# Performance work log

Hardware: AMD Instinct MI355X
Metric: run time of the kernel (lower is better)

Reference implementation:

```python
import jax, jax.numpy as jnp
import numpy as np
import math

PHI = (1.0 + math.sqrt(5.0)) / 2.0
LN_EPS = 1e-5


def _carrier_phases(n_heads: int) -> np.ndarray:
    """Reproduce DimensionalHeadManager._allocate carrier phases."""
    base = [k * math.pi / 7.0 for k in range(7)]  # rung base phases
    n_rungs = 7
    raw = []
    remaining = n_heads
    for i in range(n_rungs):
        if i < n_rungs - 1:
            c = max(1, round(n_heads / PHI ** (i + 1)))
            c = min(c, remaining - (n_rungs - 1 - i))
            raw.append(c)
            remaining -= c
        else:
            raw.append(max(1, remaining))
    phases = []
    for rung_idx, count in enumerate(raw):
        for j in range(count):
            phases.append(base[rung_idx] + 2.0 * math.pi / max(count, 1) * j)
    return np.asarray(phases[:n_heads], dtype=np.float32)


def setup_inputs() -> dict:
    key = jax.random.key(0)
    ks = jax.random.split(key, 7)
    B, S, D, H = 2, 2048, 1024, 16
    w_scale = 0.02  # realistic init scale for Linear weights
    x = jax.random.normal(ks[0], (B, S, D), dtype=jnp.float32)
    Wq = jax.random.normal(ks[1], (D, D), dtype=jnp.float32) * w_scale
    Wk = jax.random.normal(ks[2], (D, D), dtype=jnp.float32) * w_scale
    Wv = jax.random.normal(ks[3], (D, D), dtype=jnp.float32) * w_scale
    Wo = jax.random.normal(ks[4], (D, D), dtype=jnp.float32) * w_scale
    Wp = jax.random.normal(ks[5], (D,), dtype=jnp.float32) * w_scale  # W_phase (1,D) flattened
    gamma = jnp.ones((D,), dtype=jnp.float32)
    beta = jnp.zeros((D,), dtype=jnp.float32)
    carrier = jnp.asarray(_carrier_phases(H))  # srl.carrier_freq init
    lam = jnp.float32(0.1)  # lambda_resonance init
    return {"x": x, "Wq": Wq, "Wk": Wk, "Wv": Wv, "Wo": Wo, "Wp": Wp,
            "gamma": gamma, "beta": beta, "carrier": carrier, "lam": lam}


def reference(x, Wq, Wk, Wv, Wo, Wp, gamma, beta, carrier, lam):
    B, S, D = x.shape
    H = carrier.shape[0]
    dh = D // H
    scale = 1.0 / math.sqrt(dh)

    residual = x
    # LayerNorm
    mu = jnp.mean(x, axis=-1, keepdims=True)
    var = jnp.mean((x - mu) ** 2, axis=-1, keepdims=True)
    xn = (x - mu) * jax.lax.rsqrt(var + LN_EPS) * gamma + beta

    # Q/K/V projections (torch Linear: y = x @ W.T), split into heads
    q = jnp.einsum('bsd,ed->bse', xn, Wq).reshape(B, S, H, dh)
    k = jnp.einsum('bsd,ed->bse', xn, Wk).reshape(B, S, H, dh)
    v = jnp.einsum('bsd,ed->bse', xn, Wv).reshape(B, S, H, dh)

    # scalar phase per token, per-head carrier resonance gate
    phase = jnp.einsum('bsd,d->bs', xn, Wp)                       # (B,S)
    head_T = jnp.cos((phase[..., None] - carrier) * 0.5) ** 2     # (B,S,H)

    # attention scores + resonance term R_ij = cos^2((phi_i - phi_j)/2)
    scores = jnp.einsum('bihd,bjhd->bhij', q, k) * scale          # (B,H,S,S)
    R = jnp.cos((phase[:, :, None] - phase[:, None, :]) * 0.5) ** 2  # (B,S,S)
    scores = scores + lam * R[:, None, :, :]

    attn = jax.nn.softmax(scores, axis=-1)
    out = jnp.einsum('bhij,bjhd->bihd', attn, v)                  # (B,S,H,dh)
    out = out * head_T[..., None]                                 # per-head resonance gating
    emergent_energy = jnp.sum(jnp.abs(out))
    y = residual + jnp.einsum('bse,de->bsd', out.reshape(B, S, D), Wo)
    return (y, emergent_energy)
```

## Files before the change

### kernel.cpp

```cpp
#include <hip/hip_runtime.h>
#include <hip/hip_bf16.h>

#define S_LEN 2048
#define D_MODEL 1024
#define NH 16
#define DH 64
#define M_TOK 4096
#define DK 80
#define JS 2

typedef __attribute__((ext_vector_type(8))) short bf16x8;
typedef __attribute__((ext_vector_type(4))) float f32x4;
typedef __attribute__((ext_vector_type(16))) float f32x16;

#define LOG2E 1.4426950408889634f

__device__ __forceinline__ unsigned short f2bf(float f) {
  unsigned u = __float_as_uint(f);
  u += 0x7FFF + ((u >> 16) & 1);
  return (unsigned short)(u >> 16);
}

__device__ __forceinline__ void gl16(const void* g, void* l) {
  __builtin_amdgcn_global_load_lds(
      (const __attribute__((address_space(1))) unsigned int*)g,
      (__attribute__((address_space(3))) unsigned int*)l, 16, 0, 0);
}

__device__ __forceinline__ void pl32swap(unsigned int& a, unsigned int& b) {
  asm volatile("v_permlane32_swap_b32 %0, %1" : "+v"(a), "+v"(b));
}

__global__ __launch_bounds__(256) void prep_kernel(
    const float* __restrict__ Wq, const float* __restrict__ Wk,
    const float* __restrict__ Wv, const float* __restrict__ Wo,
    unsigned short* __restrict__ wbf) {
  int idx = (blockIdx.x * 256 + threadIdx.x) * 4;
  int wsel = idx >> 20;
  const float* s = (wsel == 0) ? Wq : (wsel == 1) ? Wk : (wsel == 2) ? Wv : Wo;
  int off = idx & 1048575;
  float4 v = *(const float4*)(s + off);
  ushort4 p;
  p.x = f2bf(v.x); p.y = f2bf(v.y); p.z = f2bf(v.z); p.w = f2bf(v.w);
  *(ushort4*)(wbf + idx) = p;
}

__device__ __forceinline__ float block_sum(float v, float* sm) {
#pragma unroll
  for (int o = 32; o > 0; o >>= 1) v += __shfl_xor(v, o, 64);
  int w = threadIdx.x >> 6;
  __syncthreads();
  if ((threadIdx.x & 63) == 0) sm[w] = v;
  __syncthreads();
  return sm[0] + sm[1] + sm[2] + sm[3];
}

__global__ __launch_bounds__(256) void ln_phase_kernel(
    const float* __restrict__ x, const float* __restrict__ Wp,
    const float* __restrict__ gamma, const float* __restrict__ beta,
    unsigned short* __restrict__ xn, float* __restrict__ cosP,
    float* __restrict__ sinP, unsigned short* __restrict__ kk80) {
  __shared__ float sm[4];
  int row = blockIdx.x;
  int tid = threadIdx.x;
  float4 v = ((const float4*)(x + (size_t)row * D_MODEL))[tid];
  float mu = block_sum(v.x + v.y + v.z + v.w, sm) * (1.0f / D_MODEL);
  float d0 = v.x - mu, d1 = v.y - mu, d2 = v.z - mu, d3 = v.w - mu;
  float var = block_sum(d0 * d0 + d1 * d1 + d2 * d2 + d3 * d3, sm) * (1.0f / D_MODEL);
  float rinv = rsqrtf(var + 1e-5f);
  float4 g = ((const float4*)gamma)[tid];
  float4 be = ((const float4*)beta)[tid];
  float n0 = d0 * rinv * g.x + be.x;
  float n1 = d1 * rinv * g.y + be.y;
  float n2 = d2 * rinv * g.z + be.z;
  float n3 = d3 * rinv * g.w + be.w;
  ushort4 p;
  p.x = f2bf(n0); p.y = f2bf(n1); p.z = f2bf(n2); p.w = f2bf(n3);
  ((ushort4*)(xn + (size_t)row * D_MODEL))[tid] = p;
  float4 wp = ((const float4*)Wp)[tid];
  float ph = block_sum(n0 * wp.x + n1 * wp.y + n2 * wp.z + n3 * wp.w, sm);
  if (tid == 0) {
    cosP[row] = cosf(ph);
    sinP[row] = sinf(ph);
  }
  if (tid < 16) {
    float cp = cosf(ph), sp = sinf(ph);
    unsigned int w0 = (unsigned int)f2bf(cp) | ((unsigned int)f2bf(sp) << 16);
    int b_ = row >> 11, s_ = row & (S_LEN - 1);
    *(int4*)(kk80 + ((size_t)((b_ * NH + tid) * S_LEN + s_)) * DK + 64) =
        make_int4((int)w0, 0, 0, 0);
  }
}

__global__ __launch_bounds__(256, 3) void qkv_gemm_kernel(
    const unsigned short* __restrict__ xn, const unsigned short* __restrict__ wbf,
    unsigned short* __restrict__ q, unsigned short* __restrict__ kk80,
    unsigned short* __restrict__ vT) {
  __shared__ __align__(16) unsigned short As[128 * 64];
  __shared__ __align__(16) unsigned short Bs[128 * 64];
  int bid = blockIdx.x;
  bool vmode = bid >= 512;
  const unsigned short* Ap;
  const unsigned short* Bp;
  int m0, n0;
  if (!vmode) {
    m0 = (bid >> 4) * 128;
    n0 = (bid & 15) * 128;
    Ap = xn; Bp = wbf;
  } else {
    int v2 = bid - 512;
    m0 = (v2 & 7) * 128;
    n0 = (v2 >> 3) * 128;
    Ap = wbf + 2 * D_MODEL * D_MODEL; Bp = xn;
  }
  int tid = threadIdx.x;
  int wave = tid >> 6, lane = tid & 63, quad = lane >> 4, l15 = lane & 15;
  int wm = (wave & 1) * 64, wn = (wave >> 1) * 64;
  f32x4 acc[4][4];
#pragma unroll
  for (int r = 0; r < 4; ++r)
#pragma unroll
    for (int c = 0; c < 4; ++c) acc[r][c] = (f32x4){0.f, 0.f, 0.f, 0.f};

  for (int k0 = 0; k0 < D_MODEL; k0 += 64) {
    __syncthreads();
#pragma unroll
    for (int t = 0; t < 4; ++t) {
      int c = t * 256 + tid;
      int r = c >> 3, p = c & 7;
      int g = p ^ (r & 7);
      gl16(&Ap[(size_t)(m0 + r) * D_MODEL + k0 + g * 8], &As[c * 8]);
      gl16(&Bp[(size_t)(n0 + r) * D_MODEL + k0 + g * 8], &Bs[c * 8]);
    }
    __syncthreads();
    bf16x8 af[4][2], bfr[4][2];
#pragma unroll
    for (int r = 0; r < 4; ++r) {
      int R = wm + r * 16 + l15;
#pragma unroll
      for (int h = 0; h < 2; ++h)
        af[r][h] = *(const bf16x8*)&As[R * 64 + ((h * 4 + quad) ^ (R & 7)) * 8];
    }
#pragma unroll
    for (int c = 0; c < 4; ++c) {
      int R = wn + c * 16 + l15;
#pragma unroll
      for (int h = 0; h < 2; ++h)
        bfr[c][h] = *(const bf16x8*)&Bs[R * 64 + ((h * 4 + quad) ^ (R & 7)) * 8];
    }
#pragma unroll
    for (int h = 0; h < 2; ++h)
#pragma unroll
      for (int r = 0; r < 4; ++r)
#pragma unroll
        for (int c = 0; c < 4; ++c)
          acc[r][c] = __builtin_amdgcn_mfma_f32_16x16x32_bf16(af[r][h], bfr[c][h], acc[r][c], 0, 0, 0);
  }
#pragma unroll
  for (int r = 0; r < 4; ++r) {
#pragma unroll
    for (int c = 0; c < 4; ++c) {
#pragma unroll
      for (int rr = 0; rr < 4; ++rr) {
        if (vmode) {
          int e = m0 + wm + r * 16 + quad * 4 + rr;
          int tok = n0 + wn + c * 16 + l15;
          int hh = e >> 6, d = e & 63;
          int bb = tok >> 11, ss = tok & (S_LEN - 1);
          vT[(((size_t)(bb * NH + hh)) * DH + d) * S_LEN + ss] = f2bf(acc[r][c][rr]);
        } else {
          int tok = m0 + wm + r * 16 + quad * 4 + rr;
          int n = n0 + wn + c * 16 + l15;
          int e = n & 1023;
          int hh = e >> 6, d = e & 63;
          int bb = tok >> 11, ss = tok & (S_LEN - 1);
          if ((n0 >> 10) == 0) {
            q[(((size_t)(bb * NH + hh)) * S_LEN + ss) * DH + d] =
                f2bf(acc[r][c][rr] * (0.125f * LOG2E));
          } else {
            kk80[(((size_t)(bb * NH + hh)) * S_LEN + ss) * DK + d] = f2bf(acc[r][c][rr]);
          }
        }
      }
    }
  }
}

__global__ __launch_bounds__(128, 2) void attn_kernel(
    const unsigned short* __restrict__ q, const unsigned short* __restrict__ kk80,
    const unsigned short* __restrict__ vT, const float* __restrict__ cosP,
    const float* __restrict__ sinP, const float* __restrict__ lamp,
    float* __restrict__ Opart, float* __restrict__ lpart) {
  __shared__ __align__(16) unsigned short Ks[64 * 72];
  __shared__ __align__(16) unsigned short Vs[512 * 8];
  int xx = blockIdx.x;
  int qt = xx & 15, js = xx >> 4;
  int h = blockIdx.y, b = blockIdx.z;
  int bh = b * NH + h;
  int tid = threadIdx.x, wave = tid >> 6, lane = tid & 63;
  int half = lane >> 5, l31 = lane & 31;

  const unsigned short* kb = kk80 + (size_t)bh * S_LEN * DK;
  const unsigned short* vb = vT + (size_t)bh * DH * S_LEN;
  int i0 = qt * 128 + wave * 64;

  bf16x8 bQ0[5], bQ1[5];
  {
    float hl2 = 0.5f * lamp[0] * LOG2E;
#pragma unroll
    for (int si = 0; si < 2; ++si) {
      int qrow = i0 + si * 32 + l31;
      const unsigned short* qp = q + ((size_t)bh * S_LEN + qrow) * DH;
      bf16x8* dst = si ? bQ1 : bQ0;
#pragma unroll
      for (int db = 0; db < 4; ++db)
        dst[db] = *(const bf16x8*)(qp + db * 16 + half * 8);
      bf16x8 z8 = {0, 0, 0, 0, 0, 0, 0, 0};
      if (half == 0) {
        z8[0] = (short)f2bf(hl2 * cosP[b * S_LEN + qrow]);
        z8[1] = (short)f2bf(hl2 * sinP[b * S_LEN + qrow]);
      }
      dst[4] = z8;
    }
  }

  unsigned int cc0 = tid, cc1 = tid + 128, cc2 = tid + 256, cc3 = tid + 384,
               cc4 = tid + 512;
  unsigned int kr0 = cc0 / 9u, kr1 = cc1 / 9u, kr2 = cc2 / 9u, kr3 = cc3 / 9u,
               kr4 = cc4 / 9u;
  unsigned int ko0 = kr0 * DK + (cc0 - kr0 * 9u) * 8;
  unsigned int ko1 = kr1 * DK + (cc1 - kr1 * 9u) * 8;
  unsigned int ko2 = kr2 * DK + (cc2 - kr2 * 9u) * 8;
  unsigned int ko3 = kr3 * DK + (cc3 - kr3 * 9u) * 8;
  unsigned int ko4 = kr4 * DK + (cc4 - kr4 * 9u) * 8;
  unsigned short* kl0 = (unsigned short*)Ks + cc0 * 8;
  unsigned short* kl1 = (unsigned short*)Ks + cc1 * 8;
  unsigned short* kl2 = (unsigned short*)Ks + cc2 * 8;
  unsigned short* kl3 = (unsigned short*)Ks + cc3 * 8;
  unsigned short* kl4 = (unsigned short*)Ks + cc4 * 8;
  unsigned int vr0 = cc0 >> 3, vr1 = cc1 >> 3, vr2 = cc2 >> 3, vr3 = cc3 >> 3;
  unsigned int vo0 = vr0 * S_LEN + ((cc0 & 7) ^ (vr0 & 7)) * 8;
  unsigned int vo1 = vr1 * S_LEN + ((cc1 & 7) ^ (vr1 & 7)) * 8;
  unsigned int vo2 = vr2 * S_LEN + ((cc2 & 7) ^ (vr2 & 7)) * 8;
  unsigned int vo3 = vr3 * S_LEN + ((cc3 & 7) ^ (vr3 & 7)) * 8;
  unsigned short* vl0 = (unsigned short*)Vs + cc0 * 8;
  unsigned short* vl1 = (unsigned short*)Vs + cc1 * 8;
  unsigned short* vl2 = (unsigned short*)Vs + cc2 * 8;
  unsigned short* vl3 = (unsigned short*)Vs + cc3 * 8;

  const unsigned short* kbt = kb + (size_t)(js * (S_LEN / JS)) * DK;
  const unsigned short* vbt = vb + js * (S_LEN / JS);

  f32x16 O00 = {}, O01 = {}, O10 = {}, O11 = {};
  float li0 = 0.f, li1 = 0.f;

  for (int jt = 0; jt < S_LEN / (64 * JS); ++jt) {
    __syncthreads();
    gl16(kbt + ko0, kl0);
    gl16(kbt + ko1, kl1);
    gl16(kbt + ko2, kl2);
    gl16(kbt + ko3, kl3);
    if (tid < 64) gl16(kbt + ko4, kl4);
    gl16(vbt + vo0, vl0);
    gl16(vbt + vo1, vl1);
    gl16(vbt + vo2, vl2);
    gl16(vbt + vo3, vl3);
    kbt += 64 * DK;
    vbt += 64;
    __syncthreads();

#pragma unroll
    for (int sj = 0; sj < 2; ++sj) {
      f32x16 Sf0 = {}, Sf1 = {};
      int r = sj * 32 + l31;
      __builtin_amdgcn_s_setprio(1);
#pragma unroll
      for (int db = 0; db < 5; ++db) {
        int p = (db < 4) ? (db * 2 + half) : 8;
        bf16x8 aK = *(const bf16x8*)((const unsigned short*)Ks + (r * 9 + p) * 8);
        Sf0 = __builtin_amdgcn_mfma_f32_32x32x16_bf16(aK, bQ0[db], Sf0, 0, 0, 0);
        Sf1 = __builtin_amdgcn_mfma_f32_32x32x16_bf16(aK, bQ1[db], Sf1, 0, 0, 0);
      }
      __builtin_amdgcn_s_setprio(0);

      bf16x8 pa00, pa01, pa10, pa11;
      auto smx = [&](const f32x16& S, float& li, bf16x8& pu0, bf16x8& pu1) {
        unsigned int w[8];
#pragma unroll
        for (int rr = 0; rr < 8; ++rr) {
          float e0 = exp2f(S[rr * 2 + 0]);
          float e1 = exp2f(S[rr * 2 + 1]);
          li += e0 + e1;
          __hip_bfloat162 pk2 = __float22bfloat162_rn(float2{e0, e1});
          w[rr] = *(unsigned int*)&pk2;
        }
#pragma unroll
        for (int u = 0; u < 2; ++u) {
          unsigned int a0 = w[u * 4 + 0], a1 = w[u * 4 + 1];
          unsigned int b0 = w[u * 4 + 2], b1 = w[u * 4 + 3];
          pl32swap(a0, b0);
          pl32swap(a1, b1);
          union { unsigned int u4[4]; bf16x8 v; } cvt;
          cvt.u4[0] = a0; cvt.u4[1] = a1; cvt.u4[2] = b0; cvt.u4[3] = b1;
          if (u == 0) pu0 = cvt.v; else pu1 = cvt.v;
        }
      };
      smx(Sf0, li0, pa00, pa01);
      smx(Sf1, li1, pa10, pa11);

#pragma unroll
      for (int u = 0; u < 2; ++u) {
        int jb = sj * 2 + u;
        bf16x8 paA = u ? pa01 : pa00;
        bf16x8 paB = u ? pa11 : pa10;
        __builtin_amdgcn_s_setprio(1);
        {
          int rv = l31;
          int p = (jb * 2 + half) ^ (rv & 7);
          bf16x8 bV = *(const bf16x8*)((const unsigned short*)Vs + (rv * 8 + p) * 8);
          O00 = __builtin_amdgcn_mfma_f32_32x32x16_bf16(paA, bV, O00, 0, 0, 0);
          O10 = __builtin_amdgcn_mfma_f32_32x32x16_bf16(paB, bV, O10, 0, 0, 0);
        }
        {
          int rv = 32 + l31;
          int p = (jb * 2 + half) ^ (rv & 7);
          bf16x8 bV = *(const bf16x8*)((const unsigned short*)Vs + (rv * 8 + p) * 8);
          O01 = __builtin_amdgcn_mfma_f32_32x32x16_bf16(paA, bV, O01, 0, 0, 0);
          O11 = __builtin_amdgcn_mfma_f32_32x32x16_bf16(paB, bV, O11, 0, 0, 0);
        }
        __builtin_amdgcn_s_setprio(0);
      }
    }
  }

  li0 += __shfl_xor(li0, 32, 64);
  li1 += __shfl_xor(li1, 32, 64);
  size_t obase = (size_t)(js * 2 * NH + bh) * S_LEN;
#pragma unroll
  for (int reg = 0; reg < 16; ++reg) {
    int ir = (reg & 3) + 8 * (reg >> 2) + 4 * half;
    size_t row0 = obase + i0 + ir;
    size_t row1 = obase + i0 + 32 + ir;
    Opart[row0 * DH + l31] = O00[reg];
    Opart[row0 * DH + 32 + l31] = O01[reg];
    Opart[row1 * DH + l31] = O10[reg];
    Opart[row1 * DH + 32 + l31] = O11[reg];
  }
  if (half == 0) {
    lpart[obase + i0 + l31] = li0;
    lpart[obase + i0 + 32 + l31] = li1;
  }
}

__global__ __launch_bounds__(256) void combine_kernel(
    const float* __restrict__ Opart, const float* __restrict__ lpart,
    const float* __restrict__ cosP, const float* __restrict__ sinP,
    const float* __restrict__ carrier, unsigned short* __restrict__ outw,
    float* __restrict__ earray) {
  __shared__ float sm[4];
  int tok = blockIdx.x;
  int b = tok >> 11, s = tok & (S_LEN - 1);
  int t = threadIdx.x;
  int c0 = t * 4;
  int h = c0 >> 6, d0 = c0 & 63;
  int bh = b * NH + h;
  const size_t plane = (size_t)2 * NH * S_LEN;
  size_t row0 = (size_t)bh * S_LEN + s;
  float4 a0 = *(const float4*)(Opart + row0 * DH + d0);
  float4 a1 = *(const float4*)(Opart + (plane + row0) * DH + d0);
  float l = lpart[row0] + lpart[plane + row0];
  float ch = cosf(carrier[h]), sh = sinf(carrier[h]);
  float cp = cosP[tok], sp = sinP[tok];
  float gate = 0.5f + 0.5f * (cp * ch + sp * sh);
  float gl = gate / l;
  float v0 = (a0.x + a1.x) * gl, v1 = (a0.y + a1.y) * gl;
  float v2 = (a0.z + a1.z) * gl, v3 = (a0.w + a1.w) * gl;
  ushort4 p;
  p.x = f2bf(v0); p.y = f2bf(v1); p.z = f2bf(v2); p.w = f2bf(v3);
  *(ushort4*)(outw + (size_t)tok * D_MODEL + c0) = p;
  float esum = fabsf(v0) + fabsf(v1) + fabsf(v2) + fabsf(v3);
  float tot = block_sum(esum, sm);
  if (t == 0) earray[tok] = tot;
}

__global__ __launch_bounds__(256, 3) void out_gemm_kernel(
    const unsigned short* __restrict__ A, const unsigned short* __restrict__ Wo,
    const float* __restrict__ x, const float* __restrict__ earray,
    float* __restrict__ y, float* __restrict__ energy) {
  __shared__ __align__(16) unsigned short As[128 * 64];
  __shared__ __align__(16) unsigned short Bs[128 * 64];
  __shared__ float sm[4];
  int tid = threadIdx.x;
  if (blockIdx.x == 0 && blockIdx.y == 0) {
    float v = 0.f;
#pragma unroll
    for (int i = 0; i < 16; ++i) v += earray[tid + i * 256];
    float tot = block_sum(v, sm);
    if (tid == 0) *energy = tot;
  }
  int wave = tid >> 6, lane = tid & 63, quad = lane >> 4, l15 = lane & 15;
  int wm = (wave & 1) * 64, wn = (wave >> 1) * 64;
  int m0 = blockIdx.y * 128, n0 = blockIdx.x * 128;
  f32x4 acc[4][4];
#pragma unroll
  for (int r = 0; r < 4; ++r)
#pragma unroll
    for (int c = 0; c < 4; ++c) acc[r][c] = (f32x4){0.f, 0.f, 0.f, 0.f};

  for (int k0 = 0; k0 < D_MODEL; k0 += 64) {
    __syncthreads();
#pragma unroll
    for (int t = 0; t < 4; ++t) {
      int c = t * 256 + tid;
      int r = c >> 3, p = c & 7;
      int g = p ^ (r & 7);
      gl16(&A[(size_t)(m0 + r) * D_MODEL + k0 + g * 8], &As[c * 8]);
      gl16(&Wo[(size_t)(n0 + r) * D_MODEL + k0 + g * 8], &Bs[c * 8]);
    }
    __syncthreads();
    bf16x8 af[4][2], bfr[4][2];
#pragma unroll
    for (int r = 0; r < 4; ++r) {
      int R = wm + r * 16 + l15;
#pragma unroll
      for (int h = 0; h < 2; ++h)
        af[r][h] = *(const bf16x8*)&As[R * 64 + ((h * 4 + quad) ^ (R & 7)) * 8];
    }
#pragma unroll
    for (int c = 0; c < 4; ++c) {
      int R = wn + c * 16 + l15;
#pragma unroll
      for (int h = 0; h < 2; ++h)
        bfr[c][h] = *(const bf16x8*)&Bs[R * 64 + ((h * 4 + quad) ^ (R & 7)) * 8];
    }
#pragma unroll
    for (int h = 0; h < 2; ++h)
#pragma unroll
      for (int r = 0; r < 4; ++r)
#pragma unroll
        for (int c = 0; c < 4; ++c)
          acc[r][c] = __builtin_amdgcn_mfma_f32_16x16x32_bf16(af[r][h], bfr[c][h], acc[r][c], 0, 0, 0);
  }
#pragma unroll
  for (int r = 0; r < 4; ++r) {
#pragma unroll
    for (int c = 0; c < 4; ++c) {
      int dcol = n0 + wn + c * 16 + l15;
#pragma unroll
      for (int rr = 0; rr < 4; ++rr) {
        int tok = m0 + wm + r * 16 + quad * 4 + rr;
        size_t idx = (size_t)tok * D_MODEL + dcol;
        y[idx] = x[idx] + acc[r][c][rr];
      }
    }
  }
}

extern "C" void kernel_launch(void* const* d_in, const int* in_sizes, int n_in,
                              void* d_out, int out_size, void* d_ws, size_t ws_size,
                              hipStream_t stream) {
  const float* x = (const float*)d_in[0];
  const float* Wq = (const float*)d_in[1];
  const float* Wk = (const float*)d_in[2];
  const float* Wv = (const float*)d_in[3];
  const float* Wo = (const float*)d_in[4];
  const float* Wp = (const float*)d_in[5];
  const float* gamma = (const float*)d_in[6];
  const float* beta = (const float*)d_in[7];
  const float* carrier = (const float*)d_in[8];
  const float* lam = (const float*)d_in[9];

  char* ws = (char*)d_ws;
  const size_t MB = 1024 * 1024;
  unsigned short* wbf = (unsigned short*)(ws);
  unsigned short* xn = (unsigned short*)(ws + 8 * MB);
  unsigned short* qq = (unsigned short*)(ws + 16 * MB);
  unsigned short* kk80 = (unsigned short*)(ws + 24 * MB);
  unsigned short* vT = (unsigned short*)(ws + 34 * MB);
  float* cosP = (float*)(ws + 42 * MB);
  float* sinP = (float*)(ws + 42 * MB + 16 * 1024);
  float* Opart = (float*)(ws + 43 * MB);
  float* lpart = (float*)(ws + 75 * MB);
  float* earray = (float*)(ws + 76 * MB);
  unsigned short* outw = xn;

  float* y = (float*)d_out;
  float* energy = y + (out_size - 1);

  prep_kernel<<<4096, 256, 0, stream>>>(Wq, Wk, Wv, Wo, wbf);
  ln_phase_kernel<<<M_TOK, 256, 0, stream>>>(x, Wp, gamma, beta, xn, cosP, sinP, kk80);
  qkv_gemm_kernel<<<768, 256, 0, stream>>>(xn, wbf, qq, kk80, vT);
  attn_kernel<<<dim3(16 * JS, 16, 2), 128, 0, stream>>>(qq, kk80, vT, cosP, sinP,
                                                        lam, Opart, lpart);
  combine_kernel<<<M_TOK, 256, 0, stream>>>(Opart, lpart, cosP, sinP, carrier,
                                            outw, earray);
  out_gemm_kernel<<<dim3(8, 32), 256, 0, stream>>>(outw, wbf + 3 * D_MODEL * D_MODEL,
                                                   x, earray, y, energy);
}
```

Measured before the change: 230.9 us.

## Load K/V fragments directly from global memory in attention, drop LDS staging

The attention kernel stops staging K and V tiles in shared memory and stops synchronising with barriers. Each wave now loads its MFMA operand fragments for K and V straight from global memory into registers. Blocks grow to 4 waves of 32 query rows each instead of 2 waves of 64, with launch bounds raised to 256 threads and 3 blocks per CU. This removes barrier stalls and LDS traffic, but each wave now reloads K/V on its own, which increases global/L2 traffic and leaves each wave with less reuse per load.

```diff
diff --git a/kernel.cpp b/kernel.cpp
--- a/kernel.cpp
+++ b/kernel.cpp
@@ -186,13 +186,11 @@
   }
 }
 
-__global__ __launch_bounds__(128, 2) void attn_kernel(
+__global__ __launch_bounds__(256, 3) void attn_kernel(
     const unsigned short* __restrict__ q, const unsigned short* __restrict__ kk80,
     const unsigned short* __restrict__ vT, const float* __restrict__ cosP,
     const float* __restrict__ sinP, const float* __restrict__ lamp,
     float* __restrict__ Opart, float* __restrict__ lpart) {
-  __shared__ __align__(16) unsigned short Ks[64 * 72];
-  __shared__ __align__(16) unsigned short Vs[512 * 8];
   int xx = blockIdx.x;
   int qt = xx & 15, js = xx >> 4;
   int h = blockIdx.y, b = blockIdx.z;
@@ -202,154 +200,97 @@
 
   const unsigned short* kb = kk80 + (size_t)bh * S_LEN * DK;
   const unsigned short* vb = vT + (size_t)bh * DH * S_LEN;
-  int i0 = qt * 128 + wave * 64;
-
-  bf16x8 bQ0[5], bQ1[5];
+  int i0 = qt * 128 + wave * 32;
+  int qrow = i0 + l31;
+
+  bf16x8 bQ[5];
   {
-    float hl2 = 0.5f * lamp[0] * LOG2E;
-#pragma unroll
-    for (int si = 0; si < 2; ++si) {
-      int qrow = i0 + si * 32 + l31;
-      const unsigned short* qp = q + ((size_t)bh * S_LEN + qrow) * DH;
-      bf16x8* dst = si ? bQ1 : bQ0;
-#pragma unroll
-      for (int db = 0; db < 4; ++db)
-        dst[db] = *(const bf16x8*)(qp + db * 16 + half * 8);
-      bf16x8 z8 = {0, 0, 0, 0, 0, 0, 0, 0};
-      if (half == 0) {
-        z8[0] = (short)f2bf(hl2 * cosP[b * S_LEN + qrow]);
-        z8[1] = (short)f2bf(hl2 * sinP[b * S_LEN + qrow]);
+    const unsigned short* qp = q + ((size_t)bh * S_LEN + qrow) * DH;
+#pragma unroll
+    for (int db = 0; db < 4; ++db)
+      bQ[db] = *(const bf16x8*)(qp + db * 16 + half * 8);
+    bf16x8 z8 = {0, 0, 0, 0, 0, 0, 0, 0};
+    if (half == 0) {
+      float hl2 = 0.5f * lamp[0] * LOG2E;
+      z8[0] = (short)f2bf(hl2 * cosP[b * S_LEN + qrow]);
+      z8[1] = (short)f2bf(hl2 * sinP[b * S_LEN + qrow]);
+    }
+    bQ[4] = z8;
+  }
+
+  const unsigned short* kbt0 = kb + ((size_t)(js * (S_LEN / JS)) + l31) * DK;
+  const unsigned short* kbt1 = kbt0 + 32 * DK;
+  const unsigned short* vbt0 = vb + js * (S_LEN / JS) + (size_t)l31 * S_LEN + half * 8;
+  const unsigned short* vbt1 = vbt0 + (size_t)32 * S_LEN;
+
+  f32x16 O0 = {}, O1 = {};
+  float l_i = 0.f;
+
+  for (int jt = 0; jt < S_LEN / (64 * JS); ++jt) {
+    bf16x8 aK0[5], aK1[5];
+#pragma unroll
+    for (int db = 0; db < 5; ++db) {
+      int p = (db < 4) ? (db * 2 + half) : 8;
+      aK0[db] = *(const bf16x8*)(kbt0 + p * 8);
+      aK1[db] = *(const bf16x8*)(kbt1 + p * 8);
+    }
+    bf16x8 bV0[4], bV1[4];
+#pragma unroll
+    for (int jb = 0; jb < 4; ++jb) {
+      bV0[jb] = *(const bf16x8*)(vbt0 + jb * 16);
+      bV1[jb] = *(const bf16x8*)(vbt1 + jb * 16);
+    }
+    kbt0 += 64 * DK; kbt1 += 64 * DK;
+    vbt0 += 64; vbt1 += 64;
+
+    f32x16 Sf0 = {}, Sf1 = {};
+    __builtin_amdgcn_s_setprio(1);
+#pragma unroll
+    for (int db = 0; db < 5; ++db) {
+      Sf0 = __builtin_amdgcn_mfma_f32_32x32x16_bf16(aK0[db], bQ[db], Sf0, 0, 0, 0);
+      Sf1 = __builtin_amdgcn_mfma_f32_32x32x16_bf16(aK1[db], bQ[db], Sf1, 0, 0, 0);
+    }
+    __builtin_amdgcn_s_setprio(0);
+
+#pragma unroll
+    for (int sj = 0; sj < 2; ++sj) {
+      const f32x16& S = sj ? Sf1 : Sf0;
+      unsigned int w[8];
+#pragma unroll
+      for (int rr = 0; rr < 8; ++rr) {
+        float e0 = exp2f(S[rr * 2 + 0]);
+        float e1 = exp2f(S[rr * 2 + 1]);
+        l_i += e0 + e1;
+        __hip_bfloat162 pk2 = __float22bfloat162_rn(float2{e0, e1});
+        w[rr] = *(unsigned int*)&pk2;
       }
-      dst[4] = z8;
-    }
-  }
-
-  unsigned int cc0 = tid, cc1 = tid + 128, cc2 = tid + 256, cc3 = tid + 384,
-               cc4 = tid + 512;
-  unsigned int kr0 = cc0 / 9u, kr1 = cc1 / 9u, kr2 = cc2 / 9u, kr3 = cc3 / 9u,
-               kr4 = cc4 / 9u;
-  unsigned int ko0 = kr0 * DK + (cc0 - kr0 * 9u) * 8;
-  unsigned int ko1 = kr1 * DK + (cc1 - kr1 * 9u) * 8;
-  unsigned int ko2 = kr2 * DK + (cc2 - kr2 * 9u) * 8;
-  unsigned int ko3 = kr3 * DK + (cc3 - kr3 * 9u) * 8;
-  unsigned int ko4 = kr4 * DK + (cc4 - kr4 * 9u) * 8;
-  unsigned short* kl0 = (unsigned short*)Ks + cc0 * 8;
-  unsigned short* kl1 = (unsigned short*)Ks + cc1 * 8;
-  unsigned short* kl2 = (unsigned short*)Ks + cc2 * 8;
-  unsigned short* kl3 = (unsigned short*)Ks + cc3 * 8;
-  unsigned short* kl4 = (unsigned short*)Ks + cc4 * 8;
-  unsigned int vr0 = cc0 >> 3, vr1 = cc1 >> 3, vr2 = cc2 >> 3, vr3 = cc3 >> 3;
-  unsigned int vo0 = vr0 * S_LEN + ((cc0 & 7) ^ (vr0 & 7)) * 8;
-  unsigned int vo1 = vr1 * S_LEN + ((cc1 & 7) ^ (vr1 & 7)) * 8;
-  unsigned int vo2 = vr2 * S_LEN + ((cc2 & 7) ^ (vr2 & 7)) * 8;
-  unsigned int vo3 = vr3 * S_LEN + ((cc3 & 7) ^ (vr3 & 7)) * 8;
-  unsigned short* vl0 = (unsigned short*)Vs + cc0 * 8;
-  unsigned short* vl1 = (unsigned short*)Vs + cc1 * 8;
-  unsigned short* vl2 = (unsigned short*)Vs + cc2 * 8;
-  unsigned short* vl3 = (unsigned short*)Vs + cc3 * 8;
-
-  const unsigned short* kbt = kb + (size_t)(js * (S_LEN / JS)) * DK;
-  const unsigned short* vbt = vb + js * (S_LEN / JS);
-
-  f32x16 O00 = {}, O01 = {}, O10 = {}, O11 = {};
-  float li0 = 0.f, li1 = 0.f;
-
-  for (int jt = 0; jt < S_LEN / (64 * JS); ++jt) {
-    __syncthreads();
-    gl16(kbt + ko0, kl0);
-    gl16(kbt + ko1, kl1);
-    gl16(kbt + ko2, kl2);
-    gl16(kbt + ko3, kl3);
-    if (tid < 64) gl16(kbt + ko4, kl4);
-    gl16(vbt + vo0, vl0);
-    gl16(vbt + vo1, vl1);
-    gl16(vbt + vo2, vl2);
-    gl16(vbt + vo3, vl3);
-    kbt += 64 * DK;
-    vbt += 64;
-    __syncthreads();
-
-#pragma unroll
-    for (int sj = 0; sj < 2; ++sj) {
-      f32x16 Sf0 = {}, Sf1 = {};
-      int r = sj * 32 + l31;
-      __builtin_amdgcn_s_setprio(1);
-#pragma unroll
-      for (int db = 0; db < 5; ++db) {
-        int p = (db < 4) ? (db * 2 + half) : 8;
-        bf16x8 aK = *(const bf16x8*)((const unsigned short*)Ks + (r * 9 + p) * 8);
-        Sf0 = __builtin_amdgcn_mfma_f32_32x32x16_bf16(aK, bQ0[db], Sf0, 0, 0, 0);
-        Sf1 = __builtin_amdgcn_mfma_f32_32x32x16_bf16(aK, bQ1[db], Sf1, 0, 0, 0);
-      }
-      __builtin_amdgcn_s_setprio(0);
-
-      bf16x8 pa00, pa01, pa10, pa11;
-      auto smx = [&](const f32x16& S, float& li, bf16x8& pu0, bf16x8& pu1) {
-        unsigned int w[8];
-#pragma unroll
-        for (int rr = 0; rr < 8; ++rr) {
-          float e0 = exp2f(S[rr * 2 + 0]);
-          float e1 = exp2f(S[rr * 2 + 1]);
-          li += e0 + e1;
-          __hip_bfloat162 pk2 = __float22bfloat162_rn(float2{e0, e1});
-          w[rr] = *(unsigned int*)&pk2;
-        }
-#pragma unroll
-        for (int u = 0; u < 2; ++u) {
-          unsigned int a0 = w[u * 4 + 0], a1 = w[u * 4 + 1];
-          unsigned int b0 = w[u * 4 + 2], b1 = w[u * 4 + 3];
-          pl32swap(a0, b0);
-          pl32swap(a1, b1);
-          union { unsigned int u4[4]; bf16x8 v; } cvt;
-          cvt.u4[0] = a0; cvt.u4[1] = a1; cvt.u4[2] = b0; cvt.u4[3] = b1;
-          if (u == 0) pu0 = cvt.v; else pu1 = cvt.v;
-        }
-      };
-      smx(Sf0, li0, pa00, pa01);
-      smx(Sf1, li1, pa10, pa11);
-
 #pragma unroll
       for (int u = 0; u < 2; ++u) {
+        unsigned int a0 = w[u * 4 + 0], a1 = w[u * 4 + 1];
+        unsigned int b0 = w[u * 4 + 2], b1 = w[u * 4 + 3];
+        pl32swap(a0, b0);
+        pl32swap(a1, b1);
+        union { unsigned int u4[4]; bf16x8 v; } cvt;
+        cvt.u4[0] = a0; cvt.u4[1] = a1; cvt.u4[2] = b0; cvt.u4[3] = b1;
         int jb = sj * 2 + u;
-        bf16x8 paA = u ? pa01 : pa00;
-        bf16x8 paB = u ? pa11 : pa10;
         __builtin_amdgcn_s_setprio(1);
-        {
-          int rv = l31;
-          int p = (jb * 2 + half) ^ (rv & 7);
-          bf16x8 bV = *(const bf16x8*)((const unsigned short*)Vs + (rv * 8 + p) * 8);
-          O00 = __builtin_amdgcn_mfma_f32_32x32x16_bf16(paA, bV, O00, 0, 0, 0);
-          O10 = __builtin_amdgcn_mfma_f32_32x32x16_bf16(paB, bV, O10, 0, 0, 0);
-        }
-        {
-          int rv = 32 + l31;
-          int p = (jb * 2 + half) ^ (rv & 7);
-          bf16x8 bV = *(const bf16x8*)((const unsigned short*)Vs + (rv * 8 + p) * 8);
-          O01 = __builtin_amdgcn_mfma_f32_32x32x16_bf16(paA, bV, O01, 0, 0, 0);
-          O11 = __builtin_amdgcn_mfma_f32_32x32x16_bf16(paB, bV, O11, 0, 0, 0);
-        }
+        O0 = __builtin_amdgcn_mfma_f32_32x32x16_bf16(cvt.v, bV0[jb], O0, 0, 0, 0);
+        O1 = __builtin_amdgcn_mfma_f32_32x32x16_bf16(cvt.v, bV1[jb], O1, 0, 0, 0);
         __builtin_amdgcn_s_setprio(0);
       }
     }
   }
 
-  li0 += __shfl_xor(li0, 32, 64);
-  li1 += __shfl_xor(li1, 32, 64);
+  l_i += __shfl_xor(l_i, 32, 64);
   size_t obase = (size_t)(js * 2 * NH + bh) * S_LEN;
 #pragma unroll
   for (int reg = 0; reg < 16; ++reg) {
     int ir = (reg & 3) + 8 * (reg >> 2) + 4 * half;
-    size_t row0 = obase + i0 + ir;
-    size_t row1 = obase + i0 + 32 + ir;
-    Opart[row0 * DH + l31] = O00[reg];
-    Opart[row0 * DH + 32 + l31] = O01[reg];
-    Opart[row1 * DH + l31] = O10[reg];
-    Opart[row1 * DH + 32 + l31] = O11[reg];
-  }
-  if (half == 0) {
-    lpart[obase + i0 + l31] = li0;
-    lpart[obase + i0 + 32 + l31] = li1;
-  }
+    size_t row = obase + i0 + ir;
+    Opart[row * DH + l31] = O0[reg];
+    Opart[row * DH + 32 + l31] = O1[reg];
+  }
+  if (half == 0) lpart[obase + i0 + l31] = l_i;
 }
 
 __global__ __launch_bounds__(256) void combine_kernel(
@@ -490,7 +431,7 @@
   prep_kernel<<<4096, 256, 0, stream>>>(Wq, Wk, Wv, Wo, wbf);
   ln_phase_kernel<<<M_TOK, 256, 0, stream>>>(x, Wp, gamma, beta, xn, cosP, sinP, kk80);
   qkv_gemm_kernel<<<768, 256, 0, stream>>>(xn, wbf, qq, kk80, vT);
-  attn_kernel<<<dim3(16 * JS, 16, 2), 128, 0, stream>>>(qq, kk80, vT, cosP, sinP,
+  attn_kernel<<<dim3(16 * JS, 16, 2), 256, 0, stream>>>(qq, kk80, vT, cosP, sinP,
                                                         lam, Opart, lpart);
   combine_kernel<<<M_TOK, 256, 0, stream>>>(Opart, lpart, cosP, sinP, carrier,
                                             outw, earray);
```

Result: slower. 253.7 us (+9.9%).

## Halve attention query tile per wave to double occupancy and use native exp2

Applied to the files above, without the earlier changes.

Each wave of the attention kernel now handles 32 query rows instead of 64, so the grid doubles and launch bounds request 4 blocks per CU instead of 2. This cuts accumulator register pressure to allow more resident waves. The cost is that each K/V tile loaded into LDS is reused by half as many queries, roughly doubling K/V traffic. The softmax exponential is also switched to the hardware v_exp_f32 builtin, and the row-sum is split into two accumulators.

```diff
diff --git a/kernel.cpp b/kernel.cpp
--- a/kernel.cpp
+++ b/kernel.cpp
@@ -19,6 +19,16 @@
   unsigned u = __float_as_uint(f);
   u += 0x7FFF + ((u >> 16) & 1);
   return (unsigned short)(u >> 16);
+}
+
+__device__ __forceinline__ float fexp2(float x) {
+#if __has_builtin(__builtin_amdgcn_exp2f)
+  return __builtin_amdgcn_exp2f(x);
+#else
+  float r;
+  asm("v_exp_f32 %0, %1" : "=v"(r) : "v"(x));
+  return r;
+#endif
 }
 
 __device__ __forceinline__ void gl16(const void* g, void* l) {
@@ -186,7 +196,7 @@
   }
 }
 
-__global__ __launch_bounds__(128, 2) void attn_kernel(
+__global__ __launch_bounds__(128, 4) void attn_kernel(
     const unsigned short* __restrict__ q, const unsigned short* __restrict__ kk80,
     const unsigned short* __restrict__ vT, const float* __restrict__ cosP,
     const float* __restrict__ sinP, const float* __restrict__ lamp,
@@ -194,7 +204,7 @@
   __shared__ __align__(16) unsigned short Ks[64 * 72];
   __shared__ __align__(16) unsigned short Vs[512 * 8];
   int xx = blockIdx.x;
-  int qt = xx & 15, js = xx >> 4;
+  int qt = xx & 31, js = xx >> 5;
   int h = blockIdx.y, b = blockIdx.z;
   int bh = b * NH + h;
   int tid = threadIdx.x, wave = tid >> 6, lane = tid & 63;
@@ -202,26 +212,21 @@
 
   const unsigned short* kb = kk80 + (size_t)bh * S_LEN * DK;
   const unsigned short* vb = vT + (size_t)bh * DH * S_LEN;
-  int i0 = qt * 128 + wave * 64;
-
-  bf16x8 bQ0[5], bQ1[5];
+  int qrow = qt * 64 + wave * 32 + l31;
+
+  bf16x8 bQ[5];
   {
-    float hl2 = 0.5f * lamp[0] * LOG2E;
-#pragma unroll
-    for (int si = 0; si < 2; ++si) {
-      int qrow = i0 + si * 32 + l31;
-      const unsigned short* qp = q + ((size_t)bh * S_LEN + qrow) * DH;
-      bf16x8* dst = si ? bQ1 : bQ0;
-#pragma unroll
-      for (int db = 0; db < 4; ++db)
-        dst[db] = *(const bf16x8*)(qp + db * 16 + half * 8);
-      bf16x8 z8 = {0, 0, 0, 0, 0, 0, 0, 0};
-      if (half == 0) {
-        z8[0] = (short)f2bf(hl2 * cosP[b * S_LEN + qrow]);
-        z8[1] = (short)f2bf(hl2 * sinP[b * S_LEN + qrow]);
-      }
-      dst[4] = z8;
-    }
+    const unsigned short* qp = q + ((size_t)bh * S_LEN + qrow) * DH;
+#pragma unroll
+    for (int db = 0; db < 4; ++db)
+      bQ[db] = *(const bf16x8*)(qp + db * 16 + half * 8);
+    bf16x8 z8 = {0, 0, 0, 0, 0, 0, 0, 0};
+    if (half == 0) {
+      float hl2 = 0.5f * lamp[0] * LOG2E;
+      z8[0] = (short)f2bf(hl2 * cosP[b * S_LEN + qrow]);
+      z8[1] = (short)f2bf(hl2 * sinP[b * S_LEN + qrow]);
+    }
+    bQ[4] = z8;
   }
 
   unsigned int cc0 = tid, cc1 = tid + 128, cc2 = tid + 256, cc3 = tid + 384,
@@ -251,8 +256,8 @@
   const unsigned short* kbt = kb + (size_t)(js * (S_LEN / JS)) * DK;
   const unsigned short* vbt = vb + js * (S_LEN / JS);
 
-  f32x16 O00 = {}, O01 = {}, O10 = {}, O11 = {};
-  float li0 = 0.f, li1 = 0.f;
+  f32x16 O0 = {}, O1 = {};
+  float2 l2 = {0.f, 0.f};
 
   for (int jt = 0; jt < S_LEN / (64 * JS); ++jt) {
     __syncthreads();
@@ -269,87 +274,71 @@
     vbt += 64;
     __syncthreads();
 
+    f32x16 Sf[2];
 #pragma unroll
     for (int sj = 0; sj < 2; ++sj) {
-      f32x16 Sf0 = {}, Sf1 = {};
+      Sf[sj] = (f32x16){};
       int r = sj * 32 + l31;
       __builtin_amdgcn_s_setprio(1);
 #pragma unroll
       for (int db = 0; db < 5; ++db) {
         int p = (db < 4) ? (db * 2 + half) : 8;
         bf16x8 aK = *(const bf16x8*)((const unsigned short*)Ks + (r * 9 + p) * 8);
-        Sf0 = __builtin_amdgcn_mfma_f32_32x32x16_bf16(aK, bQ0[db], Sf0, 0, 0, 0);
-        Sf1 = __builtin_amdgcn_mfma_f32_32x32x16_bf16(aK, bQ1[db], Sf1, 0, 0, 0);
+        Sf[sj] = __builtin_amdgcn_mfma_f32_32x32x16_bf16(aK, bQ[db], Sf[sj], 0, 0, 0);
       }
       __builtin_amdgcn_s_setprio(0);
-
-      bf16x8 pa00, pa01, pa10, pa11;
-      auto smx = [&](const f32x16& S, float& li, bf16x8& pu0, bf16x8& pu1) {
-        unsigned int w[8];
-#pragma unroll
-        for (int rr = 0; rr < 8; ++rr) {
-          float e0 = exp2f(S[rr * 2 + 0]);
-          float e1 = exp2f(S[rr * 2 + 1]);
-          li += e0 + e1;
-          __hip_bfloat162 pk2 = __float22bfloat162_rn(float2{e0, e1});
-          w[rr] = *(unsigned int*)&pk2;
-        }
-#pragma unroll
-        for (int u = 0; u < 2; ++u) {
-          unsigned int a0 = w[u * 4 + 0], a1 = w[u * 4 + 1];
-          unsigned int b0 = w[u * 4 + 2], b1 = w[u * 4 + 3];
-          pl32swap(a0, b0);
-          pl32swap(a1, b1);
-          union { unsigned int u4[4]; bf16x8 v; } cvt;
-          cvt.u4[0] = a0; cvt.u4[1] = a1; cvt.u4[2] = b0; cvt.u4[3] = b1;
-          if (u == 0) pu0 = cvt.v; else pu1 = cvt.v;
-        }
-      };
-      smx(Sf0, li0, pa00, pa01);
-      smx(Sf1, li1, pa10, pa11);
-
+    }
+
+#pragma unroll
+    for (int sj = 0; sj < 2; ++sj) {
+      unsigned int w[8];
+#pragma unroll
+      for (int rr = 0; rr < 8; ++rr) {
+        float e0 = fexp2(Sf[sj][rr * 2 + 0]);
+        float e1 = fexp2(Sf[sj][rr * 2 + 1]);
+        l2.x += e0;
+        l2.y += e1;
+        __hip_bfloat162 pk2 = __float22bfloat162_rn(float2{e0, e1});
+        w[rr] = *(unsigned int*)&pk2;
+      }
 #pragma unroll
       for (int u = 0; u < 2; ++u) {
+        unsigned int a0 = w[u * 4 + 0], a1 = w[u * 4 + 1];
+        unsigned int b0 = w[u * 4 + 2], b1 = w[u * 4 + 3];
+        pl32swap(a0, b0);
+        pl32swap(a1, b1);
+        union { unsigned int u4[4]; bf16x8 v; } cvt;
+        cvt.u4[0] = a0; cvt.u4[1] = a1; cvt.u4[2] = b0; cvt.u4[3] = b1;
         int jb = sj * 2 + u;
-        bf16x8 paA = u ? pa01 : pa00;
-        bf16x8 paB = u ? pa11 : pa10;
         __builtin_amdgcn_s_setprio(1);
         {
           int rv = l31;
           int p = (jb * 2 + half) ^ (rv & 7);
           bf16x8 bV = *(const bf16x8*)((const unsigned short*)Vs + (rv * 8 + p) * 8);
-          O00 = __builtin_amdgcn_mfma_f32_32x32x16_bf16(paA, bV, O00, 0, 0, 0);
-          O10 = __builtin_amdgcn_mfma_f32_32x32x16_bf16(paB, bV, O10, 0, 0, 0);
+          O0 = __builtin_amdgcn_mfma_f32_32x32x16_bf16(cvt.v, bV, O0, 0, 0, 0);
         }
         {
           int rv = 32 + l31;
           int p = (jb * 2 + half) ^ (rv & 7);
           bf16x8 bV = *(const bf16x8*)((const unsigned short*)Vs + (rv * 8 + p) * 8);
-          O01 = __builtin_amdgcn_mfma_f32_32x32x16_bf16(paA, bV, O01, 0, 0, 0);
-          O11 = __builtin_amdgcn_mfma_f32_32x32x16_bf16(paB, bV, O11, 0, 0, 0);
+          O1 = __builtin_amdgcn_mfma_f32_32x32x16_bf16(cvt.v, bV, O1, 0, 0, 0);
         }
         __builtin_amdgcn_s_setprio(0);
       }
     }
   }
 
-  li0 += __shfl_xor(li0, 32, 64);
-  li1 += __shfl_xor(li1, 32, 64);
+  float l_i = l2.x + l2.y;
+  l_i += __shfl_xor(l_i, 32, 64);
   size_t obase = (size_t)(js * 2 * NH + bh) * S_LEN;
 #pragma unroll
   for (int reg = 0; reg < 16; ++reg) {
     int ir = (reg & 3) + 8 * (reg >> 2) + 4 * half;
-    size_t row0 = obase + i0 + ir;
-    size_t row1 = obase + i0 + 32 + ir;
-    Opart[row0 * DH + l31] = O00[reg];
-    Opart[row0 * DH + 32 + l31] = O01[reg];
-    Opart[row1 * DH + l31] = O10[reg];
-    Opart[row1 * DH + 32 + l31] = O11[reg];
-  }
-  if (half == 0) {
-    lpart[obase + i0 + l31] = li0;
-    lpart[obase + i0 + 32 + l31] = li1;
-  }
+    int srow = qt * 64 + wave * 32 + ir;
+    Opart[((size_t)(obase + srow)) * DH + l31] = O0[reg];
+    Opart[((size_t)(obase + srow)) * DH + 32 + l31] = O1[reg];
+  }
+  if (half == 0) lpart[obase + qt * 64 + wave * 32 + l31] = l_i;
 }
 
 __global__ __launch_bounds__(256) void combine_kernel(
@@ -490,7 +479,7 @@
   prep_kernel<<<4096, 256, 0, stream>>>(Wq, Wk, Wv, Wo, wbf);
   ln_phase_kernel<<<M_TOK, 256, 0, stream>>>(x, Wp, gamma, beta, xn, cosP, sinP, kk80);
   qkv_gemm_kernel<<<768, 256, 0, stream>>>(xn, wbf, qq, kk80, vT);
-  attn_kernel<<<dim3(16 * JS, 16, 2), 128, 0, stream>>>(qq, kk80, vT, cosP, sinP,
+  attn_kernel<<<dim3(32 * JS, 16, 2), 128, 0, stream>>>(qq, kk80, vT, cosP, sinP,
                                                         lam, Opart, lpart);
   combine_kernel<<<M_TOK, 256, 0, stream>>>(Opart, lpart, cosP, sinP, carrier,
                                             outw, earray);
```

Result: faster. 222.1 us (-3.8%).
